# Performance work log

Measured on AMD Instinct MI355X. Metric: run time of the kernel, lower is better.

Reference implementation:

```python
import jax, jax.numpy as jnp
import numpy as np

H = W = 512
MAX_ID = 15          # instance ids 1..15 (0 = background)
N_SIGMA = 1
FG_WEIGHT = 1.0
W_INST, W_VAR, W_SEED = 1.0, 10.0, 1.0


def make_xym(h, w):
    # channel 0 varies along width (x), channel 1 along height (y), like the torch buffer
    xs = jnp.linspace(0.0, 1.0, 512)
    xm = jnp.broadcast_to(xs[None, None, :], (1, 512, 512))
    ym = jnp.broadcast_to(xs[None, :, None], (1, 512, 512))
    xym = jnp.concatenate([xm, ym], axis=0)
    return xym[:, :h, :w]


def lovasz_hinge_flat(logits, labels):
    # logits, labels: flat [P]; labels in {0,1} float
    signs = 2.0 * labels - 1.0
    errors = 1.0 - logits * signs
    perm = jnp.argsort(-errors)                 # descending
    errors_sorted = errors[perm]
    gt_sorted = labels[perm]
    gts = jnp.sum(gt_sorted)
    intersection = gts - jnp.cumsum(gt_sorted)
    union = gts + jnp.cumsum(1.0 - gt_sorted)
    jaccard = 1.0 - intersection / union
    jaccard = jnp.concatenate([jaccard[:1], jaccard[1:] - jaccard[:-1]])
    return jnp.sum(jax.nn.relu(errors_sorted) * jaccard)


def _per_image(pred_b, inst_b, lab_b, xym):
    spatial_emb = jnp.tanh(pred_b[0:2]) + xym          # (2,H,W)
    sigma = pred_b[2]                                  # (H,W), n_sigma=1
    seed_map = jax.nn.sigmoid(pred_b[3])               # (H,W)

    bg = (lab_b == 0)
    seed_bg = jnp.sum(jnp.where(bg, seed_map ** 2, 0.0))

    def per_inst(iid):
        m = (inst_b == iid).astype(pred_b.dtype)       # (H,W)
        cnt = jnp.sum(m)
        present = cnt > 0
        cnt_s = jnp.maximum(cnt, 1.0)
        # to_center=True: center from coordinate map
        center = jnp.sum(xym * m[None], axis=(1, 2)) / cnt_s            # (2,)
        sig_mean = jnp.sum(sigma * m) / cnt_s
        var_l = jnp.sum((sigma - jax.lax.stop_gradient(sig_mean)) ** 2 * m) / cnt_s
        s = jnp.exp(sig_mean * 10.0)
        d2 = jnp.sum((spatial_emb - center[:, None, None]) ** 2, axis=0)  # (H,W)
        dist = jnp.exp(-d2 * s)
        inst_l = lovasz_hinge_flat(dist.reshape(-1) * 2.0 - 1.0, m.reshape(-1))
        seed_l = jnp.sum((seed_map - jax.lax.stop_gradient(dist)) ** 2 * m)
        intra_l = 1.0 - jnp.sum(dist * m) / cnt_s
        return present, var_l, inst_l, seed_l, intra_l

    ids = jnp.arange(1, MAX_ID + 1)
    present, var_l, inst_l, seed_l, intra_l = jax.vmap(per_inst)(ids)
    pf = present.astype(pred_b.dtype)
    obj = jnp.sum(pf)
    obj_s = jnp.maximum(obj, 1.0)
    instance_loss = jnp.sum(inst_l * pf) / obj_s
    var_loss = jnp.sum(var_l * pf) / obj_s
    intra_loss = jnp.sum(intra_l * pf)          # NOT divided by obj_count (as in source)
    seed_loss = (seed_bg + FG_WEIGHT * jnp.sum(seed_l * pf)) / (H * W)
    return W_INST * instance_loss + W_VAR * var_loss + W_SEED * seed_loss + 5.0 * intra_loss


def setup_inputs() -> dict:
    key = jax.random.key(0)
    k1, k2, k3 = jax.random.split(key, 3)
    prediction = jax.random.normal(k1, (4, 4, H, W), dtype=jnp.float32)
    instances = jax.random.randint(k2, (4, H, W), 0, MAX_ID + 1, dtype=jnp.int32)
    labels = jax.random.randint(k3, (4, H, W), 0, 2, dtype=jnp.int32)
    return {"prediction": prediction, "instances": instances, "labels": labels}


def reference(prediction, instances, labels):
    xym = make_xym(prediction.shape[2], prediction.shape[3])
    per_b = jax.vmap(_per_image, in_axes=(0, 0, 0, None))(prediction, instances, labels, xym)
    return jnp.mean(per_b)
```

## Files before the change

### kernel.cpp

```cpp
#include <hip/hip_runtime.h>

#define HW     262144
#define NB     4
#define NID    15
#define KB     256
#define CHUNKS 128
#define PXC    (HW / CHUNKS)

#define WS_STATR  0
#define WS_SEEDBG 1024
#define WS_ACCR   1028
#define WS_LOV    1796
#define WS_CTRL   2048
#define WS_HIST   2048
#define HIST_U32  (NB * CHUNKS * NID * KB * 2)
#define WS_EMBX   (WS_HIST + HIST_U32)
#define MAP_SZ    (NB * HW)
#define WS_EMBY   (WS_EMBX + MAP_SZ)
#define WS_SEEDM  (WS_EMBY + MAP_SZ)
#define WS_TOTAL  (WS_SEEDM + MAP_SZ)

__device__ __forceinline__ float rcp_fast(float x) { return __builtin_amdgcn_rcpf(x); }
__device__ __forceinline__ float fast_tanh(float x) {
    return 1.0f - 2.0f * rcp_fast(__expf(2.0f * x) + 1.0f);
}
__device__ __forceinline__ float fast_sigmoid(float x) {
    return rcp_fast(1.0f + __expf(-x));
}

__global__ __launch_bounds__(256) void prepKernel(const float* __restrict__ pred,
                                                  const int* __restrict__ inst,
                                                  const int* __restrict__ lab,
                                                  float* __restrict__ ws) {
    __shared__ float s_acc[16][68];
    const int b   = blockIdx.y;
    const int tid = threadIdx.x;
    for (int j = tid; j < 16 * 68; j += 256) ((float*)s_acc)[j] = 0.f;
    __syncthreads();

    const int grp = tid >> 4;
    const int ib = b * HW;
    const float* p0 = pred + (((size_t)(b * 4 + 0)) << 18);
    const float* p1 = pred + (((size_t)(b * 4 + 1)) << 18);
    const float* p2 = pred + (((size_t)(b * 4 + 2)) << 18);
    const float* p3 = pred + (((size_t)(b * 4 + 3)) << 18);
    float* embx  = ws + WS_EMBX + ib;
    float* emby  = ws + WS_EMBY + ib;
    float* seedm = ws + WS_SEEDM + ib;
    const float inv511 = 1.0f / 511.0f;

    const int p = blockIdx.x * 1024 + tid * 4;
    const int4   i4 = *(const int4*)(inst + ib + p);
    const int4   l4 = *(const int4*)(lab + ib + p);
    const float4 a4 = *(const float4*)(p0 + p);
    const float4 b4 = *(const float4*)(p1 + p);
    const float4 g4 = *(const float4*)(p2 + p);
    const float4 t4 = *(const float4*)(p3 + p);
    const float xs0 = (float)(p & 511) * inv511;
    const float ys  = (float)(p >> 9) * inv511;

    float4 ex, ey, sd;
    ex.x = fast_tanh(a4.x) + xs0;
    ex.y = fast_tanh(a4.y) + xs0 + inv511;
    ex.z = fast_tanh(a4.z) + xs0 + 2.f * inv511;
    ex.w = fast_tanh(a4.w) + xs0 + 3.f * inv511;
    ey.x = fast_tanh(b4.x) + ys;
    ey.y = fast_tanh(b4.y) + ys;
    ey.z = fast_tanh(b4.z) + ys;
    ey.w = fast_tanh(b4.w) + ys;
    sd.x = fast_sigmoid(t4.x);
    sd.y = fast_sigmoid(t4.y);
    sd.z = fast_sigmoid(t4.z);
    sd.w = fast_sigmoid(t4.w);
    *(float4*)(embx + p)  = ex;
    *(float4*)(emby + p)  = ey;
    *(float4*)(seedm + p) = sd;

    float sbg = 0.f;
    sbg += (l4.x == 0) ? sd.x * sd.x : 0.f;
    sbg += (l4.y == 0) ? sd.y * sd.y : 0.f;
    sbg += (l4.z == 0) ? sd.z * sd.z : 0.f;
    sbg += (l4.w == 0) ? sd.w * sd.w : 0.f;

#define ACC_PX(IID, XS, SG)                                   \
    if ((IID) > 0) {                                          \
        float* a = &s_acc[grp][((IID) - 1) * 4];              \
        atomicAdd(a + 0, 1.f);                                \
        atomicAdd(a + 1, (XS));                               \
        atomicAdd(a + 2, ys);                                 \
        atomicAdd(a + 3, (SG));                               \
    }
    ACC_PX(i4.x, xs0, g4.x)
    ACC_PX(i4.y, xs0 + inv511, g4.y)
    ACC_PX(i4.z, xs0 + 2.f * inv511, g4.z)
    ACC_PX(i4.w, xs0 + 3.f * inv511, g4.w)
#undef ACC_PX

#pragma unroll
    for (int m = 32; m; m >>= 1) sbg += __shfl_xor(sbg, m, 64);
    if ((tid & 63) == 0) atomicAdd(&s_acc[grp][60], sbg);
    __syncthreads();

    if (tid < 61) {
        float tot = 0.f;
#pragma unroll
        for (int q = 0; q < 16; ++q) tot += s_acc[q][tid];
        if (tid < 60) atomicAdd(ws + WS_STATR + (blockIdx.x & 3) * 256 + b * 60 + tid, tot);
        else          atomicAdd(ws + WS_SEEDBG + b, tot);
    }
}

__global__ __launch_bounds__(256) void histKernel(const float* __restrict__ pred,
                                                  const int* __restrict__ inst,
                                                  float* __restrict__ ws) {
    __shared__ unsigned s_hist[NID][KB * 2];
    __shared__ float4   s_stat4[NID];
    __shared__ float    s_facc[16][48];

    const int b     = blockIdx.y;
    const int chunk = blockIdx.x;
    const int tid   = threadIdx.x;

    if (tid < NID) {
        float cnt = 0.f, sx = 0.f, sy = 0.f, ss = 0.f;
#pragma unroll
        for (int r = 0; r < 4; ++r) {
            const float* st = ws + WS_STATR + r * 256 + b * 60 + tid * 4;
            cnt += st[0]; sx += st[1]; sy += st[2]; ss += st[3];
        }
        float ic = rcp_fast(fmaxf(cnt, 1.f));
        float sigm = ss * ic;
        s_stat4[tid] = make_float4(sx * ic, sy * ic, sigm, __expf(10.f * sigm));
    }
    for (int j = tid; j < NID * KB * 2; j += 256) ((unsigned*)s_hist)[j] = 0u;
    for (int j = tid; j < 16 * 48; j += 256) ((float*)s_facc)[j] = 0.f;
    __syncthreads();

    float csx[NID], csy[NID], css[NID];
#pragma unroll
    for (int i = 0; i < NID; ++i) {
        float4 v = s_stat4[i];
        csx[i] = v.x; csy[i] = v.y; css[i] = v.w;
    }

    const int grp = tid >> 4;
    const int ib = b * HW;
    const float* sig   = pred + (((size_t)(b * 4 + 2)) << 18);
    const float* embx  = ws + WS_EMBX + ib;
    const float* emby  = ws + WS_EMBY + ib;
    const float* seedm = ws + WS_SEEDM + ib;

    auto doPx = [&](float exv, float eyv, float sdv, float gv, int iid) {
#pragma unroll
        for (int i = 0; i < NID; ++i) {
            float dx = exv - csx[i], dy = eyv - csy[i];
            float dist = __expf(-(dx * dx + dy * dy) * css[i]);
            float u1 = dist * (float)KB;
            bool m = (iid == i + 1);
            float bf = m ? ((float)KB - u1) : u1;
            int bk = min((int)bf, KB - 1);
            atomicAdd(&s_hist[i][bk * 2 + (m ? 0 : 1)], 1u);
        }
        if (iid > 0) {
            float4 st = s_stat4[iid - 1];
            float dx = exv - st.x, dy = eyv - st.y;
            float dist = __expf(-(dx * dx + dy * dy) * st.w);
            float dsg = gv - st.z;
            float e2 = sdv - dist;
            float* fa = &s_facc[grp][(iid - 1) * 3];
            atomicAdd(fa + 0, dsg * dsg);
            atomicAdd(fa + 1, e2 * e2);
            atomicAdd(fa + 2, dist);
        }
    };

#pragma unroll
    for (int u = 0; u < 2; ++u) {
        const int p = chunk * PXC + u * 1024 + tid * 4;
        const int4   i4 = *(const int4*)(inst + ib + p);
        const float4 exq = *(const float4*)(embx + p);
        const float4 eyq = *(const float4*)(emby + p);
        const float4 sdq = *(const float4*)(seedm + p);
        const float4 gq  = *(const float4*)(sig + p);
        doPx(exq.x, eyq.x, sdq.x, gq.x, i4.x);
        doPx(exq.y, eyq.y, sdq.y, gq.y, i4.y);
        doPx(exq.z, eyq.z, sdq.z, gq.z, i4.z);
        doPx(exq.w, eyq.w, sdq.w, gq.w, i4.w);
    }
    __syncthreads();

    unsigned* dst = (unsigned*)(ws + WS_HIST) + (size_t)(b * CHUNKS + chunk) * (NID * KB * 2);
    const uint4* src4 = (const uint4*)s_hist;
    uint4* dst4 = (uint4*)dst;
    for (int j = tid; j < NID * KB * 2 / 4; j += 256) dst4[j] = src4[j];

    if (tid < 45) {
        float tot = 0.f;
#pragma unroll
        for (int q = 0; q < 16; ++q) tot += s_facc[q][tid];
        atomicAdd(ws + WS_ACCR + (chunk & 3) * 192 + b * 48 + tid, tot);
    }
}

__global__ __launch_bounds__(64) void lovaszKernel(float* __restrict__ ws) {
    const int t = blockIdx.x;
    const int lane = threadIdx.x;
    const int b = t / NID, i = t % NID;
    float G = 0.f;
#pragma unroll
    for (int r = 0; r < 4; ++r) G += ws[WS_STATR + r * 256 + b * 60 + i * 4];

    float sum = 0.f;
    if (G > 0.f) {
        const unsigned* histU = (const unsigned*)(ws + WS_HIST);
        unsigned a0 = 0, a1 = 0, a2 = 0, a3 = 0, a4 = 0, a5 = 0, a6 = 0, a7 = 0;
        for (int c = 0; c < CHUNKS; ++c) {
            const unsigned* hb = histU + ((size_t)(b * CHUNKS + c) * NID + i) * (KB * 2) + lane * 8;
            uint4 q0 = *(const uint4*)(hb);
            uint4 q1 = *(const uint4*)(hb + 4);
            a0 += q0.x; a1 += q0.y; a2 += q0.z; a3 += q0.w;
            a4 += q1.x; a5 += q1.y; a6 += q1.z; a7 += q1.w;
        }
        float fgs[4] = {(float)a0, (float)a2, (float)a4, (float)a6};
        float bgs[4] = {(float)a1, (float)a3, (float)a5, (float)a7};
        float Fl = fgs[0] + fgs[1] + fgs[2] + fgs[3];
        float Bl = bgs[0] + bgs[1] + bgs[2] + bgs[3];
        float Fs = Fl, Bs = Bl;
#pragma unroll
        for (int d = 1; d < 64; d <<= 1) {
            float fu = __shfl_down(Fs, d, 64);
            float bu = __shfl_down(Bs, d, 64);
            if (lane + d < 64) { Fs += fu; Bs += bu; }
        }
        float F = Fs - Fl, B = Bs - Bl;
        float Jprev = 1.f - (G - F) * rcp_fast(G + B);
        const float ew = 2.f / (float)KB;
#pragma unroll
        for (int q = 3; q >= 0; --q) {
            F += fgs[q]; B += bgs[q];
            float J = 1.f - (G - F) * rcp_fast(G + B);
            float ek = ((float)(lane * 4 + q) + 0.5f) * ew;
            sum += ek * (J - Jprev);
            Jprev = J;
        }
#pragma unroll
        for (int m = 32; m; m >>= 1) sum += __shfl_xor(sum, m, 64);
    }
    if (lane == 0) ws[WS_LOV + t] = sum;
}

__global__ __launch_bounds__(64) void finalKernel(const float* __restrict__ ws,
                                                  float* __restrict__ out) {
    __shared__ float s_c[60][5];
    const int tid = threadIdx.x;
    if (tid < 60) {
        const int b = tid / NID, i = tid % NID;
        float cnt = 0.f, v = 0.f, sdl = 0.f, dm = 0.f;
#pragma unroll
        for (int r = 0; r < 4; ++r) {
            cnt += ws[WS_STATR + r * 256 + b * 60 + i * 4];
            const float* ac = ws + WS_ACCR + r * 192 + b * 48 + i * 3;
            v += ac[0]; sdl += ac[1]; dm += ac[2];
        }
        float pf = cnt > 0.f ? 1.f : 0.f;
        float ic = cnt > 0.f ? 1.f / cnt : 0.f;
        s_c[tid][0] = pf;
        s_c[tid][1] = pf * ws[WS_LOV + tid];
        s_c[tid][2] = pf * v * ic;
        s_c[tid][3] = pf * (1.f - dm * ic);
        s_c[tid][4] = pf * sdl;
    }
    __syncthreads();
    if (tid == 0) {
        float total = 0.f;
        for (int b = 0; b < NB; ++b) {
            float obj = 0.f, instl = 0.f, varl = 0.f, intral = 0.f, seedl = 0.f;
            for (int i = 0; i < NID; ++i) {
                const float* r = s_c[b * NID + i];
                obj += r[0]; instl += r[1]; varl += r[2]; intral += r[3]; seedl += r[4];
            }
            float objs = fmaxf(obj, 1.f);
            total += instl / objs
                   + 10.f * (varl / objs)
                   + (ws[WS_SEEDBG + b] + seedl) / (float)HW
                   + 5.f * intral;
        }
        out[0] = total * 0.25f;
    }
}

extern "C" void kernel_launch(void* const* d_in, const int* in_sizes, int n_in,
                              void* d_out, int out_size, void* d_ws, size_t ws_size,
                              hipStream_t stream) {
    const float* pred = (const float*)d_in[0];
    const int*   inst = (const int*)d_in[1];
    const int*   lab  = (const int*)d_in[2];
    float* ws  = (float*)d_ws;
    float* out = (float*)d_out;

    hipMemsetAsync(d_ws, 0, WS_CTRL * sizeof(float), stream);
    prepKernel<<<dim3(256, NB), 256, 0, stream>>>(pred, inst, lab, ws);
    histKernel<<<dim3(CHUNKS, NB), 256, 0, stream>>>(pred, inst, ws);
    lovaszKernel<<<60, 64, 0, stream>>>(ws);
    finalKernel<<<1, 64, 0, stream>>>(ws, out);
}
```

Before: 86.60 us.

## Pack fg/bg histogram counts into 16-bit halves with replicated LDS copies

Histogram bins now store foreground counts in the low 16 bits and background counts in the high 16 bits of one word. This halves the shared histogram and the global per-chunk histogram traffic. Four replicated LDS copies, reduced at write-out, are meant to lower atomic contention. The lovasz kernel now spreads the chunk reduction over four waves, and the memset is replaced with a small zero kernel. The packing relies on per-chunk counts per bin staying below 65536, which holds since each chunk has 2048 pixels.

```diff
diff --git a/kernel.cpp b/kernel.cpp
--- a/kernel.cpp
+++ b/kernel.cpp
@@ -13,7 +13,7 @@
 #define WS_LOV    1796
 #define WS_CTRL   2048
 #define WS_HIST   2048
-#define HIST_U32  (NB * CHUNKS * NID * KB * 2)
+#define HIST_U32  (NB * CHUNKS * NID * KB)
 #define WS_EMBX   (WS_HIST + HIST_U32)
 #define MAP_SZ    (NB * HW)
 #define WS_EMBY   (WS_EMBX + MAP_SZ)
@@ -26,6 +26,10 @@
 }
 __device__ __forceinline__ float fast_sigmoid(float x) {
     return rcp_fast(1.0f + __expf(-x));
+}
+
+__global__ __launch_bounds__(256) void zeroKernel(float* __restrict__ ws) {
+    ws[blockIdx.x * 256 + threadIdx.x] = 0.f;
 }
 
 __global__ __launch_bounds__(256) void prepKernel(const float* __restrict__ pred,
@@ -110,12 +114,13 @@
     }
 }
 
+#define HCOPY_STRIDE (NID * KB + 1)
 __global__ __launch_bounds__(256) void histKernel(const float* __restrict__ pred,
                                                   const int* __restrict__ inst,
                                                   float* __restrict__ ws) {
-    __shared__ unsigned s_hist[NID][KB * 2];
+    __shared__ unsigned s_hist[4 * HCOPY_STRIDE];
     __shared__ float4   s_stat4[NID];
-    __shared__ float    s_facc[16][48];
+    __shared__ float    s_facc[8][48];
 
     const int b     = blockIdx.y;
     const int chunk = blockIdx.x;
@@ -132,8 +137,8 @@
         float sigm = ss * ic;
         s_stat4[tid] = make_float4(sx * ic, sy * ic, sigm, __expf(10.f * sigm));
     }
-    for (int j = tid; j < NID * KB * 2; j += 256) ((unsigned*)s_hist)[j] = 0u;
-    for (int j = tid; j < 16 * 48; j += 256) ((float*)s_facc)[j] = 0.f;
+    for (int j = tid; j < 4 * HCOPY_STRIDE; j += 256) s_hist[j] = 0u;
+    for (int j = tid; j < 8 * 48; j += 256) ((float*)s_facc)[j] = 0.f;
     __syncthreads();
 
     float csx[NID], csy[NID], css[NID];
@@ -143,7 +148,8 @@
         csx[i] = v.x; csy[i] = v.y; css[i] = v.w;
     }
 
-    const int grp = tid >> 4;
+    unsigned* myhist = &s_hist[((tid >> 4) & 3) * HCOPY_STRIDE];
+    float* myfacc = s_facc[(tid >> 3) & 7];
     const int ib = b * HW;
     const float* sig   = pred + (((size_t)(b * 4 + 2)) << 18);
     const float* embx  = ws + WS_EMBX + ib;
@@ -159,7 +165,7 @@
             bool m = (iid == i + 1);
             float bf = m ? ((float)KB - u1) : u1;
             int bk = min((int)bf, KB - 1);
-            atomicAdd(&s_hist[i][bk * 2 + (m ? 0 : 1)], 1u);
+            atomicAdd(&myhist[i * KB + bk], m ? 1u : 0x10000u);
         }
         if (iid > 0) {
             float4 st = s_stat4[iid - 1];
@@ -167,7 +173,7 @@
             float dist = __expf(-(dx * dx + dy * dy) * st.w);
             float dsg = gv - st.z;
             float e2 = sdv - dist;
-            float* fa = &s_facc[grp][(iid - 1) * 3];
+            float* fa = &myfacc[(iid - 1) * 3];
             atomicAdd(fa + 0, dsg * dsg);
             atomicAdd(fa + 1, e2 * e2);
             atomicAdd(fa + 2, dist);
@@ -189,40 +195,60 @@
     }
     __syncthreads();
 
-    unsigned* dst = (unsigned*)(ws + WS_HIST) + (size_t)(b * CHUNKS + chunk) * (NID * KB * 2);
-    const uint4* src4 = (const uint4*)s_hist;
-    uint4* dst4 = (uint4*)dst;
-    for (int j = tid; j < NID * KB * 2 / 4; j += 256) dst4[j] = src4[j];
+    unsigned* dst = (unsigned*)(ws + WS_HIST) + (size_t)(b * CHUNKS + chunk) * (NID * KB);
+    for (int j = tid; j < NID * KB; j += 256) {
+        dst[j] = s_hist[j] + s_hist[HCOPY_STRIDE + j] +
+                 s_hist[2 * HCOPY_STRIDE + j] + s_hist[3 * HCOPY_STRIDE + j];
+    }
 
     if (tid < 45) {
         float tot = 0.f;
 #pragma unroll
-        for (int q = 0; q < 16; ++q) tot += s_facc[q][tid];
+        for (int q = 0; q < 8; ++q) tot += s_facc[q][tid];
         atomicAdd(ws + WS_ACCR + (chunk & 3) * 192 + b * 48 + tid, tot);
     }
 }
 
-__global__ __launch_bounds__(64) void lovaszKernel(float* __restrict__ ws) {
+__global__ __launch_bounds__(256) void lovaszKernel(float* __restrict__ ws) {
+    __shared__ unsigned s_pf[4][KB];
+    __shared__ unsigned s_pb[4][KB];
     const int t = blockIdx.x;
-    const int lane = threadIdx.x;
     const int b = t / NID, i = t % NID;
+    const int tid = threadIdx.x, wv = tid >> 6, lane = tid & 63;
+
     float G = 0.f;
 #pragma unroll
     for (int r = 0; r < 4; ++r) G += ws[WS_STATR + r * 256 + b * 60 + i * 4];
 
+    if (G > 0.f) {
+        unsigned af0 = 0, af1 = 0, af2 = 0, af3 = 0;
+        unsigned ab0 = 0, ab1 = 0, ab2 = 0, ab3 = 0;
+        const unsigned* histU = (const unsigned*)(ws + WS_HIST);
+        for (int k = 0; k < 32; ++k) {
+            const int c = wv * 32 + k;
+            const unsigned* hb = histU + ((size_t)(b * CHUNKS + c) * NID + i) * KB + lane * 4;
+            uint4 q = *(const uint4*)hb;
+            af0 += q.x & 0xffffu; ab0 += q.x >> 16;
+            af1 += q.y & 0xffffu; ab1 += q.y >> 16;
+            af2 += q.z & 0xffffu; ab2 += q.z >> 16;
+            af3 += q.w & 0xffffu; ab3 += q.w >> 16;
+        }
+        s_pf[wv][lane * 4 + 0] = af0; s_pb[wv][lane * 4 + 0] = ab0;
+        s_pf[wv][lane * 4 + 1] = af1; s_pb[wv][lane * 4 + 1] = ab1;
+        s_pf[wv][lane * 4 + 2] = af2; s_pb[wv][lane * 4 + 2] = ab2;
+        s_pf[wv][lane * 4 + 3] = af3; s_pb[wv][lane * 4 + 3] = ab3;
+    }
+    __syncthreads();
+
     float sum = 0.f;
-    if (G > 0.f) {
-        const unsigned* histU = (const unsigned*)(ws + WS_HIST);
-        unsigned a0 = 0, a1 = 0, a2 = 0, a3 = 0, a4 = 0, a5 = 0, a6 = 0, a7 = 0;
-        for (int c = 0; c < CHUNKS; ++c) {
-            const unsigned* hb = histU + ((size_t)(b * CHUNKS + c) * NID + i) * (KB * 2) + lane * 8;
-            uint4 q0 = *(const uint4*)(hb);
-            uint4 q1 = *(const uint4*)(hb + 4);
-            a0 += q0.x; a1 += q0.y; a2 += q0.z; a3 += q0.w;
-            a4 += q1.x; a5 += q1.y; a6 += q1.z; a7 += q1.w;
-        }
-        float fgs[4] = {(float)a0, (float)a2, (float)a4, (float)a6};
-        float bgs[4] = {(float)a1, (float)a3, (float)a5, (float)a7};
+    if (wv == 0 && G > 0.f) {
+        float fgs[4], bgs[4];
+#pragma unroll
+        for (int q = 0; q < 4; ++q) {
+            int k = lane * 4 + q;
+            fgs[q] = (float)(s_pf[0][k] + s_pf[1][k] + s_pf[2][k] + s_pf[3][k]);
+            bgs[q] = (float)(s_pb[0][k] + s_pb[1][k] + s_pb[2][k] + s_pb[3][k]);
+        }
         float Fl = fgs[0] + fgs[1] + fgs[2] + fgs[3];
         float Bl = bgs[0] + bgs[1] + bgs[2] + bgs[3];
         float Fs = Fl, Bs = Bl;
@@ -246,7 +272,7 @@
 #pragma unroll
         for (int m = 32; m; m >>= 1) sum += __shfl_xor(sum, m, 64);
     }
-    if (lane == 0) ws[WS_LOV + t] = sum;
+    if (tid == 0) ws[WS_LOV + t] = sum;
 }
 
 __global__ __launch_bounds__(64) void finalKernel(const float* __restrict__ ws,
@@ -298,9 +324,9 @@
     float* ws  = (float*)d_ws;
     float* out = (float*)d_out;
 
-    hipMemsetAsync(d_ws, 0, WS_CTRL * sizeof(float), stream);
+    zeroKernel<<<WS_CTRL / 256, 256, 0, stream>>>(ws);
     prepKernel<<<dim3(256, NB), 256, 0, stream>>>(pred, inst, lab, ws);
     histKernel<<<dim3(CHUNKS, NB), 256, 0, stream>>>(pred, inst, ws);
-    lovaszKernel<<<60, 64, 0, stream>>>(ws);
+    lovaszKernel<<<60, 256, 0, stream>>>(ws);
     finalKernel<<<1, 64, 0, stream>>>(ws, out);
 }
```

Measured after the change: 79.68 us. -8.0%, faster.
